# Performance work log

Hardware: AMD Instinct MI355X
Metric: run time of the kernel (lower is better)

The kernel has to match this reference:

```python
import jax, jax.numpy as jnp
import numpy as np

K = 5
PAD = 2  # same-size output: pad = dilation*(k-1)/2


def _patches(x, k, pad):
    # x: [B, C, H, W] -> [B, C, k, k, H', W'] (matches torch F.unfold + view layout)
    B, C, H, W = x.shape
    p = jax.lax.conv_general_dilated_patches(
        x, (k, k), (1, 1), [(pad, pad), (pad, pad)])
    return p.reshape(B, C, k, k, p.shape[-2], p.shape[-1])


def setup_inputs() -> dict:
    key = jax.random.key(0)
    k1, k2, k3, k4 = jax.random.split(key, 4)
    B, Cin, Cout, Cg, H, W = 4, 32, 32, 8, 128, 128
    x = jax.random.normal(k1, (B, Cin, H, W), jnp.float32)
    guide = jax.random.normal(k2, (B, Cg, H, W), jnp.float32)
    weight = jax.random.normal(k3, (Cout, Cin, K, K), jnp.float32) * 0.05
    bias = jax.random.normal(k4, (Cout,), jnp.float32) * 0.05
    return {"x": x, "guide": guide, "weight": weight, "bias": bias}


def reference(x, guide, weight, bias):
    k = weight.shape[-1]
    # --- packernel2d (gaussian, smooth_kernel_type='none', channel_wise=False) ---
    gp = _patches(guide, k, PAD)                      # [B, Cg, k, k, H, W]
    center = gp[:, :, k // 2, k // 2][:, :, None, None]  # self-tap feature
    d = gp - center
    kernel = jnp.exp(-0.5 * jnp.sum(d * d, axis=1, keepdims=True))  # [B,1,k,k,H,W]
    # --- pacconv2d native path ---
    cols = _patches(x, k, PAD)                        # [B, Cin, k, k, H, W]
    out = jnp.einsum('bjklmn,ojkl->bomn', cols * kernel, weight)
    return out + bias[None, :, None, None]
```

## Files before the change

kernel.cpp:

```cpp
#include <hip/hip_runtime.h>

#define Bn   4
#define CIN  32
#define COUT 32
#define CG   8
#define Hh   128
#define Ww   128
#define KK   5
#define HW   (Hh * Ww)

#define TW   64
#define TH   4
#define PRW  68
#define PRH  8
#define NSLOT (PRW * PRH)

#define PADW 132

typedef _Float16 h8  __attribute__((ext_vector_type(8)));
typedef _Float16 h2  __attribute__((ext_vector_type(2)));
typedef float    f4  __attribute__((ext_vector_type(4)));

#define XOFF  0
#define XJG   8704
#define WOFF  34816
#define KOFF  60416
#define SMEMB 73216

#define XT_OFF 0
#define WT_OFF 4460544
#define GT_OFF 4511744
#define WS_NEED 5560320

#define GLDS(gp, lp) __builtin_amdgcn_global_load_lds( \
    (const __attribute__((address_space(1))) void*)(gp), \
    (__attribute__((address_space(3))) void*)(lp), 16, 0, 0)

__global__ __launch_bounds__(512) void prep(
    const float* __restrict__ x, const float* __restrict__ guide,
    const float* __restrict__ w,
    _Float16* __restrict__ xt, _Float16* __restrict__ wt, _Float16* __restrict__ gt)
{
    const int bid = blockIdx.x;
    const int tid = threadIdx.x;

    if (bid < 512) {
        const int b = bid >> 7, m = bid & 127;
        const int n = tid & 127, jh = tid >> 7;
        const float* xp = x + ((size_t)(b * CIN + jh * 8)) * HW + m * Ww + n;
        h8 v;
#pragma unroll
        for (int e = 0; e < 8; ++e) v[e] = (_Float16)xp[(size_t)e * HW];
        ((h8*)xt)[(((size_t)b * PADW + m + 2) * PADW + n + 2) * 4 + jh] = v;
    } else if (bid < 562) {
        const int idx = (bid - 512) * 512 + tid;
        const int ht = idx >> 9;
        const int half = ht / 25, t = ht - half * 25;
        const int rem = idx & 511;
        const int jg = rem >> 7, o = (rem >> 3) & 15, e = rem & 7;
        wt[idx] = (_Float16)w[(size_t)(half * 16 + o) * (CIN * KK * KK) + (jg * 8 + e) * (KK * KK) + t];
    } else if (bid < 690) {
        const int gr = (bid - 562) * 4 + (tid >> 7);
        const int b = gr >> 7, m = gr & 127;
        const int n = tid & 127;
        const float* gp = guide + ((size_t)b * CG) * HW + m * Ww + n;
        h8 v;
#pragma unroll
        for (int e = 0; e < 8; ++e) v[e] = (_Float16)gp[(size_t)e * HW];
        ((h8*)gt)[(size_t)b * HW + m * Ww + n] = v;
    } else {
        const int idx = (bid - 690) * 512 + tid;
        if (idx < 4160) {
            const int b = idx / 1040, r = idx - b * 1040;
            int mp, np;
            if (r < 528) {
                const int mr = r / 132;
                mp = (mr < 2) ? mr : mr + 128;
                np = r - mr * 132;
            } else {
                const int r2 = r - 528;
                mp = 2 + (r2 >> 2);
                const int q = r2 & 3;
                np = (q < 2) ? q : q + 128;
            }
            h8 z = {};
            h8* dst = (h8*)xt + (((size_t)b * PADW + mp) * PADW + np) * 4;
            dst[0] = z; dst[1] = z; dst[2] = z; dst[3] = z;
        }
    }
}

__global__ __launch_bounds__(512, 2) void pac_mfma10(
    const _Float16* __restrict__ xt, const _Float16* __restrict__ wt,
    const _Float16* __restrict__ gt, const float* __restrict__ bias,
    float* __restrict__ out)
{
    __shared__ __align__(16) unsigned char smem[SMEMB];

    const int tid = threadIdx.x;
    const int bx  = blockIdx.x;
    const int bz  = blockIdx.y;
    const int tm = (bx >> 1) * TH;
    const int tn = (bx & 1) * TW;

    const int lane = tid & 63;
    const int l15 = lane & 15, kg = lane >> 4;
    const int wv = tid >> 6;

    for (int c = wv; c < 34; c += 8) {
        const int i = c * 64 + lane;
        const int jg = i / NSLOT;
        const int slot = i - jg * NSLOT;
        const int r = slot / PRW, cc = slot - r * PRW;
        const _Float16* g = xt +
            ((((size_t)bz * PADW + tm + r) * PADW + tn + cc) * 4 + jg) * 8;
        GLDS(g, smem + XOFF + c * 1024);
    }

    for (int c = wv; c < 25; c += 8) {
        const _Float16* g = wt + (c * 64 + lane) * 8;
        GLDS(g, smem + WOFF + c * 1024);
    }

    const h8* wh1 = (const h8*)wt + 1600;
    h8 B1r[25];
#pragma unroll
    for (int t = 0; t < 25; ++t)
        B1r[t] = wh1[t * 64 + kg * 16 + l15];

    {
        const int px = tid & 255, th = tid >> 8;
        const int pr = px >> 6, pc = px & 63;
        const int pg = px >> 5, ps = (px >> 4) & 1, pi = px & 15;
        const int m = tm + pr, n = tn + pc;
        const h8* gtb = (const h8*)gt + (size_t)bz * HW;
        const h8 c8 = gtb[m * Ww + n];
        float cg[8];
#pragma unroll
        for (int i = 0; i < 8; ++i) cg[i] = (float)c8[i];
        int t = 0;
#pragma unroll
        for (int k = 0; k < KK; ++k) {
#pragma unroll
            for (int l = 0; l < KK; ++l) {
                if ((t < 13) == (th == 0)) {
                    const int gm = m + k - 2, gn = n + l - 2;
                    h8 gv = {};
                    if ((unsigned)gm < (unsigned)Hh && (unsigned)gn < (unsigned)Ww)
                        gv = gtb[gm * Ww + gn];
                    float ss = 0.f;
#pragma unroll
                    for (int i = 0; i < 8; ++i) {
                        const float d = (float)gv[i] - cg[i];
                        ss = fmaf(d, d, ss);
                    }
                    *(_Float16*)(smem + KOFF + t * 512 + ((pg * 16 + pi) * 2 + ps) * 2) =
                        (_Float16)__expf(-0.5f * ss);
                }
                ++t;
            }
        }
    }

    __syncthreads();

    const int st0 = wv * 32, st1 = st0 + 16;
    const int r0 = wv >> 1;
    const int c00 = (wv & 1) * 32;

    f4 acc00 = {0.f,0.f,0.f,0.f}, acc01 = {0.f,0.f,0.f,0.f};
    f4 acc10 = {0.f,0.f,0.f,0.f}, acc11 = {0.f,0.f,0.f,0.f};
    const unsigned char* xg = smem + XOFF + kg * XJG;
    const int kbase = KOFF + (wv * 16 + l15) * 4;

    int t = 0;
#pragma unroll
    for (int k = 0; k < KK; ++k) {
#pragma unroll
        for (int l = 0; l < KK; ++l) {
            const int abase = ((r0 + k) * PRW + c00 + l + l15) * 16;
            h8 A0 = *(const h8*)(xg + abase);
            h8 A1 = *(const h8*)(xg + abase + 256);
            h8 B0 = *(const h8*)(smem + WOFF + t * 1024 + kg * 256 + l15 * 16);
            h2 kk = *(const h2*)(smem + kbase + t * 512);

            h8 A0s = A0 * kk[0];
            h8 A1s = A1 * kk[1];

            acc00 = __builtin_amdgcn_mfma_f32_16x16x32_f16(A0s, B0,     acc00, 0, 0, 0);
            acc01 = __builtin_amdgcn_mfma_f32_16x16x32_f16(A0s, B1r[t], acc01, 0, 0, 0);
            acc10 = __builtin_amdgcn_mfma_f32_16x16x32_f16(A1s, B0,     acc10, 0, 0, 0);
            acc11 = __builtin_amdgcn_mfma_f32_16x16x32_f16(A1s, B1r[t], acc11, 0, 0, 0);
            ++t;
        }
    }

    const float bv0 = bias[l15], bv1 = bias[16 + l15];
#pragma unroll
    for (int i = 0; i < 4; ++i) {
        acc00[i] += bv0; acc10[i] += bv0;
        acc01[i] += bv1; acc11[i] += bv1;
    }

    __syncthreads();
    float* outst = (float*)smem;
    *(f4*)(outst + l15 * 260 + st0 + kg * 4) = acc00;
    *(f4*)(outst + l15 * 260 + st1 + kg * 4) = acc10;
    *(f4*)(outst + (16 + l15) * 260 + st0 + kg * 4) = acc01;
    *(f4*)(outst + (16 + l15) * 260 + st1 + kg * 4) = acc11;
    __syncthreads();

    const int o = tid >> 4;
    const int i = tid & 15;
    float* op = out + ((size_t)(bz * COUT + o)) * HW;
#pragma unroll
    for (int c = 0; c < 4; ++c) {
        f4 v = *(const f4*)(outst + o * 260 + c * 64 + i * 4);
        *(f4*)(op + (size_t)(tm + c) * Ww + tn + i * 4) = v;
    }
}

typedef _Float16 h4v __attribute__((ext_vector_type(4)));
__global__ __launch_bounds__(512, 4) void pac_mfma2(
    const float* __restrict__ x, const float* __restrict__ guide,
    const float* __restrict__ weight, const float* __restrict__ bias,
    float* __restrict__ out)
{
    __shared__ __align__(16) unsigned char smem[SMEMB];
    const int tid  = threadIdx.x;
    const int bx   = blockIdx.x;
    const int half = blockIdx.y;
    const int bz   = blockIdx.z;
    const int tm = (bx >> 1) * TH;
    const int tn = (bx & 1) * TW;

    const float* xb = x + (size_t)bz * CIN * HW;
#pragma unroll
    for (int it = 0; it < 34; ++it) {
        const int idx  = it * 512 + tid;
        const int j    = idx / NSLOT;
        const int slot = idx - j * NSLOT;
        const int r    = slot / PRW;
        const int c    = slot - r * PRW;
        const int gm = tm + r - 2, gn = tn + c - 2;
        float v = 0.f;
        if ((unsigned)gm < (unsigned)Hh && (unsigned)gn < (unsigned)Ww)
            v = xb[(size_t)j * HW + gm * Ww + gn];
        *(_Float16*)(smem + XOFF + (j >> 3) * XJG + slot * 16 + (j & 7) * 2) = (_Float16)v;
    }
#pragma unroll
    for (int it = 0; it < 25; ++it) {
        const int idx = it * 512 + tid;
        const int o = idx & 15;
        const int j = (idx >> 4) & 31;
        const int t = idx >> 9;
        const float v = weight[(size_t)(half * 16 + o) * (CIN * KK * KK) + j * (KK * KK) + t];
        *(_Float16*)(smem + WOFF + t * 1024 + (j >> 3) * 256 + o * 16 + (j & 7) * 2) = (_Float16)v;
    }
    {
        const int px = tid & 255, th = tid >> 8;
        const int pr = px >> 6, pc = px & 63;
        const int m = tm + pr, n = tn + pc;
        const float* gb = guide + ((size_t)bz * CG) * HW + m * Ww + n;
        float center[CG];
#pragma unroll
        for (int c = 0; c < CG; ++c) center[c] = gb[c * HW];
        int t = 0;
#pragma unroll
        for (int k = 0; k < KK; ++k) {
            const int dm = k - 2;
            const bool rowok = ((unsigned)(m + dm) < (unsigned)Hh);
#pragma unroll
            for (int l = 0; l < KK; ++l) {
                if ((t < 13) == (th == 0)) {
                    const int dn = l - 2;
                    const bool ok = rowok && ((unsigned)(n + dn) < (unsigned)Ww);
                    float ss = 0.f;
#pragma unroll
                    for (int c = 0; c < CG; ++c) {
                        float gv = ok ? gb[c * HW + dm * Ww + dn] : 0.f;
                        float d = gv - center[c];
                        ss = fmaf(d, d, ss);
                    }
                    *(_Float16*)(smem + KOFF + t * 512 + px * 2) = (_Float16)__expf(-0.5f * ss);
                }
                ++t;
            }
        }
    }
    __syncthreads();
    const int lane = tid & 63;
    const int l15 = lane & 15, kg = lane >> 4;
    const int wv = tid >> 6;
    const int st0 = wv * 32, st1 = st0 + 16;
    const int r0 = wv >> 1;
    const int c00 = (wv & 1) * 32;
    f4 acc0 = {0.f, 0.f, 0.f, 0.f}, acc1 = {0.f, 0.f, 0.f, 0.f};
    const unsigned char* xg = smem + XOFF + kg * XJG;
    const float bv = bias[half * 16 + l15];
    int t = 0;
#pragma unroll
    for (int k = 0; k < KK; ++k) {
#pragma unroll
        for (int l = 0; l < KK; ++l) {
            const int abase = ((r0 + k) * PRW + c00 + l + l15) * 16;
            h8 A0 = *(const h8*)(xg + abase);
            h8 A1 = *(const h8*)(xg + abase + 256);
            h8 Bv = *(const h8*)(smem + WOFF + t * 1024 + kg * 256 + l15 * 16);
            f4 p0 = __builtin_amdgcn_mfma_f32_16x16x32_f16(A0, Bv, (f4){0.f,0.f,0.f,0.f}, 0, 0, 0);
            f4 p1 = __builtin_amdgcn_mfma_f32_16x16x32_f16(A1, Bv, (f4){0.f,0.f,0.f,0.f}, 0, 0, 0);
            h4v k0 = *(const h4v*)(smem + KOFF + t * 512 + (st0 + kg * 4) * 2);
            h4v k1 = *(const h4v*)(smem + KOFF + t * 512 + (st1 + kg * 4) * 2);
#pragma unroll
            for (int i = 0; i < 4; ++i) {
                acc0[i] = fmaf((float)k0[i], p0[i], acc0[i]);
                acc1[i] = fmaf((float)k1[i], p1[i], acc1[i]);
            }
            ++t;
        }
    }
#pragma unroll
    for (int i = 0; i < 4; ++i) { acc0[i] += bv; acc1[i] += bv; }
    __syncthreads();
    float* outst = (float*)smem;
    *(f4*)(outst + l15 * 260 + st0 + kg * 4) = acc0;
    *(f4*)(outst + l15 * 260 + st1 + kg * 4) = acc1;
    __syncthreads();
    const int o = tid >> 5;
    const int p = (tid & 31) * 8;
    f4 v0 = *(const f4*)(outst + o * 260 + p);
    f4 v1 = *(const f4*)(outst + o * 260 + p + 4);
    const int mr = p >> 6, nc = p & 63;
    float* op = out + ((size_t)(bz * COUT + half * 16 + o)) * HW + (size_t)(tm + mr) * Ww + tn + nc;
    *(f4*)op = v0;
    *(f4*)(op + 4) = v1;
}

extern "C" void kernel_launch(void* const* d_in, const int* in_sizes, int n_in,
                              void* d_out, int out_size, void* d_ws, size_t ws_size,
                              hipStream_t stream) {
    const float* x      = (const float*)d_in[0];
    const float* guide  = (const float*)d_in[1];
    const float* weight = (const float*)d_in[2];
    const float* bias   = (const float*)d_in[3];
    float* out = (float*)d_out;

    if (ws_size >= (size_t)WS_NEED) {
        _Float16* xt = (_Float16*)((char*)d_ws + XT_OFF);
        _Float16* wt = (_Float16*)((char*)d_ws + WT_OFF);
        _Float16* gt = (_Float16*)((char*)d_ws + GT_OFF);
        prep<<<dim3(699), 512, 0, stream>>>(x, guide, weight, xt, wt, gt);
        pac_mfma10<<<dim3(64, Bn), 512, 0, stream>>>(xt, wt, gt, bias, out);
    } else {
        pac_mfma2<<<dim3(64, 2, Bn), 512, 0, stream>>>(x, guide, weight, bias, out);
    }
}
```

Before: 23.57 us.

## Double block to 1024 threads with one 16-pixel tile per wave

The main fused kernel now runs 16 waves per block instead of 8. Each wave computes one 16-pixel by 32-output tile (two MFMAs per tap) instead of a 32-pixel tile with four MFMAs. Both weight halves are now staged in LDS rather than the second half being held in 25 registers per lane, and the gaussian kernel computation is split across four thread groups. The aim is to cut register pressure and raise the number of waves available to hide latency. The cost is larger LDS use per block (about 99KB), which may limit residency to one block per CU, and weight reads now come from LDS instead of registers.

```diff
diff --git a/kernel.cpp b/kernel.cpp
--- a/kernel.cpp
+++ b/kernel.cpp
@@ -18,14 +18,13 @@
 #define PADW 132
 
 typedef _Float16 h8  __attribute__((ext_vector_type(8)));
-typedef _Float16 h2  __attribute__((ext_vector_type(2)));
 typedef float    f4  __attribute__((ext_vector_type(4)));
 
 #define XOFF  0
 #define XJG   8704
 #define WOFF  34816
-#define KOFF  60416
-#define SMEMB 73216
+#define KOFF  86016
+#define SMEMB 98816
 
 #define XT_OFF 0
 #define WT_OFF 4460544
@@ -90,7 +89,7 @@
     }
 }
 
-__global__ __launch_bounds__(512, 2) void pac_mfma10(
+__global__ __launch_bounds__(1024, 4) void pac_mfma11(
     const _Float16* __restrict__ xt, const _Float16* __restrict__ wt,
     const _Float16* __restrict__ gt, const float* __restrict__ bias,
     float* __restrict__ out)
@@ -107,7 +106,7 @@
     const int l15 = lane & 15, kg = lane >> 4;
     const int wv = tid >> 6;
 
-    for (int c = wv; c < 34; c += 8) {
+    for (int c = wv; c < 34; c += 16) {
         const int i = c * 64 + lane;
         const int jg = i / NSLOT;
         const int slot = i - jg * NSLOT;
@@ -117,21 +116,15 @@
         GLDS(g, smem + XOFF + c * 1024);
     }
 
-    for (int c = wv; c < 25; c += 8) {
+    for (int c = wv; c < 50; c += 16) {
         const _Float16* g = wt + (c * 64 + lane) * 8;
         GLDS(g, smem + WOFF + c * 1024);
     }
 
-    const h8* wh1 = (const h8*)wt + 1600;
-    h8 B1r[25];
-#pragma unroll
-    for (int t = 0; t < 25; ++t)
-        B1r[t] = wh1[t * 64 + kg * 16 + l15];
-
     {
         const int px = tid & 255, th = tid >> 8;
+        const int lo = (th * 25) >> 2, hi = ((th + 1) * 25) >> 2;
         const int pr = px >> 6, pc = px & 63;
-        const int pg = px >> 5, ps = (px >> 4) & 1, pi = px & 15;
         const int m = tm + pr, n = tn + pc;
         const h8* gtb = (const h8*)gt + (size_t)bz * HW;
         const h8 c8 = gtb[m * Ww + n];
@@ -143,7 +136,7 @@
         for (int k = 0; k < KK; ++k) {
 #pragma unroll
             for (int l = 0; l < KK; ++l) {
-                if ((t < 13) == (th == 0)) {
+                if (t >= lo && t < hi) {
                     const int gm = m + k - 2, gn = n + l - 2;
                     h8 gv = {};
                     if ((unsigned)gm < (unsigned)Hh && (unsigned)gn < (unsigned)Ww)
@@ -154,7 +147,7 @@
                         const float d = (float)gv[i] - cg[i];
                         ss = fmaf(d, d, ss);
                     }
-                    *(_Float16*)(smem + KOFF + t * 512 + ((pg * 16 + pi) * 2 + ps) * 2) =
+                    *(_Float16*)(smem + KOFF + t * 512 + px * 2) =
                         (_Float16)__expf(-0.5f * ss);
                 }
                 ++t;
@@ -164,69 +157,62 @@
 
     __syncthreads();
 
-    const int st0 = wv * 32, st1 = st0 + 16;
-    const int r0 = wv >> 1;
-    const int c00 = (wv & 1) * 32;
-
-    f4 acc00 = {0.f,0.f,0.f,0.f}, acc01 = {0.f,0.f,0.f,0.f};
-    f4 acc10 = {0.f,0.f,0.f,0.f}, acc11 = {0.f,0.f,0.f,0.f};
+    const int st0 = wv * 16;
+    const int r0 = wv >> 2;
+    const int c0 = (wv & 3) * 16;
+
+    f4 acc0 = {0.f,0.f,0.f,0.f}, acc1 = {0.f,0.f,0.f,0.f};
     const unsigned char* xg = smem + XOFF + kg * XJG;
-    const int kbase = KOFF + (wv * 16 + l15) * 4;
 
     int t = 0;
 #pragma unroll
     for (int k = 0; k < KK; ++k) {
 #pragma unroll
         for (int l = 0; l < KK; ++l) {
-            const int abase = ((r0 + k) * PRW + c00 + l + l15) * 16;
+            const int abase = ((r0 + k) * PRW + c0 + l + l15) * 16;
             h8 A0 = *(const h8*)(xg + abase);
-            h8 A1 = *(const h8*)(xg + abase + 256);
             h8 B0 = *(const h8*)(smem + WOFF + t * 1024 + kg * 256 + l15 * 16);
-            h2 kk = *(const h2*)(smem + kbase + t * 512);
-
-            h8 A0s = A0 * kk[0];
-            h8 A1s = A1 * kk[1];
-
-            acc00 = __builtin_amdgcn_mfma_f32_16x16x32_f16(A0s, B0,     acc00, 0, 0, 0);
-            acc01 = __builtin_amdgcn_mfma_f32_16x16x32_f16(A0s, B1r[t], acc01, 0, 0, 0);
-            acc10 = __builtin_amdgcn_mfma_f32_16x16x32_f16(A1s, B0,     acc10, 0, 0, 0);
-            acc11 = __builtin_amdgcn_mfma_f32_16x16x32_f16(A1s, B1r[t], acc11, 0, 0, 0);
+            h8 B1 = *(const h8*)(smem + WOFF + 25600 + t * 1024 + kg * 256 + l15 * 16);
+            const _Float16 kk = *(const _Float16*)(smem + KOFF + t * 512 + (st0 + l15) * 2);
+
+            h8 A0s = A0 * kk;
+
+            acc0 = __builtin_amdgcn_mfma_f32_16x16x32_f16(A0s, B0, acc0, 0, 0, 0);
+            acc1 = __builtin_amdgcn_mfma_f32_16x16x32_f16(A0s, B1, acc1, 0, 0, 0);
             ++t;
         }
     }
 
     const float bv0 = bias[l15], bv1 = bias[16 + l15];
 #pragma unroll
-    for (int i = 0; i < 4; ++i) {
-        acc00[i] += bv0; acc10[i] += bv0;
-        acc01[i] += bv1; acc11[i] += bv1;
-    }
+    for (int i = 0; i < 4; ++i) { acc0[i] += bv0; acc1[i] += bv1; }
 
     __syncthreads();
     float* outst = (float*)smem;
-    *(f4*)(outst + l15 * 260 + st0 + kg * 4) = acc00;
-    *(f4*)(outst + l15 * 260 + st1 + kg * 4) = acc10;
-    *(f4*)(outst + (16 + l15) * 260 + st0 + kg * 4) = acc01;
-    *(f4*)(outst + (16 + l15) * 260 + st1 + kg * 4) = acc11;
-    __syncthreads();
-
-    const int o = tid >> 4;
-    const int i = tid & 15;
-    float* op = out + ((size_t)(bz * COUT + o)) * HW;
-#pragma unroll
-    for (int c = 0; c < 4; ++c) {
-        f4 v = *(const f4*)(outst + o * 260 + c * 64 + i * 4);
-        *(f4*)(op + (size_t)(tm + c) * Ww + tn + i * 4) = v;
-    }
+    *(f4*)(outst + l15 * 260 + st0 + kg * 4) = acc0;
+    *(f4*)(outst + (16 + l15) * 260 + st0 + kg * 4) = acc1;
+    __syncthreads();
+
+    const int o = tid >> 5;
+    const int p = (tid & 31) * 8;
+    const int row = p >> 6, col = p & 63;
+    float* op = out + ((size_t)(bz * COUT + o)) * HW + (size_t)(tm + row) * Ww + tn + col;
+    const float* src = outst + o * 260 + p;
+    *(f4*)op = *(const f4*)src;
+    *(f4*)(op + 4) = *(const f4*)(src + 4);
 }
 
 typedef _Float16 h4v __attribute__((ext_vector_type(4)));
+#define FXOFF  0
+#define FXJG   8704
+#define FWOFF  34816
+#define FKOFF  60416
 __global__ __launch_bounds__(512, 4) void pac_mfma2(
     const float* __restrict__ x, const float* __restrict__ guide,
     const float* __restrict__ weight, const float* __restrict__ bias,
     float* __restrict__ out)
 {
-    __shared__ __align__(16) unsigned char smem[SMEMB];
+    __shared__ __align__(16) unsigned char smem[73216];
     const int tid  = threadIdx.x;
     const int bx   = blockIdx.x;
     const int half = blockIdx.y;
@@ -246,7 +232,7 @@
         float v = 0.f;
         if ((unsigned)gm < (unsigned)Hh && (unsigned)gn < (unsigned)Ww)
             v = xb[(size_t)j * HW + gm * Ww + gn];
-        *(_Float16*)(smem + XOFF + (j >> 3) * XJG + slot * 16 + (j & 7) * 2) = (_Float16)v;
+        *(_Float16*)(smem + FXOFF + (j >> 3) * FXJG + slot * 16 + (j & 7) * 2) = (_Float16)v;
     }
 #pragma unroll
     for (int it = 0; it < 25; ++it) {
@@ -255,7 +241,7 @@
         const int j = (idx >> 4) & 31;
         const int t = idx >> 9;
         const float v = weight[(size_t)(half * 16 + o) * (CIN * KK * KK) + j * (KK * KK) + t];
-        *(_Float16*)(smem + WOFF + t * 1024 + (j >> 3) * 256 + o * 16 + (j & 7) * 2) = (_Float16)v;
+        *(_Float16*)(smem + FWOFF + t * 1024 + (j >> 3) * 256 + o * 16 + (j & 7) * 2) = (_Float16)v;
     }
     {
         const int px = tid & 255, th = tid >> 8;
@@ -282,7 +268,7 @@
                         float d = gv - center[c];
                         ss = fmaf(d, d, ss);
                     }
-                    *(_Float16*)(smem + KOFF + t * 512 + px * 2) = (_Float16)__expf(-0.5f * ss);
+                    *(_Float16*)(smem + FKOFF + t * 512 + px * 2) = (_Float16)__expf(-0.5f * ss);
                 }
                 ++t;
             }
@@ -296,7 +282,7 @@
     const int r0 = wv >> 1;
     const int c00 = (wv & 1) * 32;
     f4 acc0 = {0.f, 0.f, 0.f, 0.f}, acc1 = {0.f, 0.f, 0.f, 0.f};
-    const unsigned char* xg = smem + XOFF + kg * XJG;
+    const unsigned char* xg = smem + FXOFF + kg * FXJG;
     const float bv = bias[half * 16 + l15];
     int t = 0;
 #pragma unroll
@@ -306,11 +292,11 @@
             const int abase = ((r0 + k) * PRW + c00 + l + l15) * 16;
             h8 A0 = *(const h8*)(xg + abase);
             h8 A1 = *(const h8*)(xg + abase + 256);
-            h8 Bv = *(const h8*)(smem + WOFF + t * 1024 + kg * 256 + l15 * 16);
+            h8 Bv = *(const h8*)(smem + FWOFF + t * 1024 + kg * 256 + l15 * 16);
             f4 p0 = __builtin_amdgcn_mfma_f32_16x16x32_f16(A0, Bv, (f4){0.f,0.f,0.f,0.f}, 0, 0, 0);
             f4 p1 = __builtin_amdgcn_mfma_f32_16x16x32_f16(A1, Bv, (f4){0.f,0.f,0.f,0.f}, 0, 0, 0);
-            h4v k0 = *(const h4v*)(smem + KOFF + t * 512 + (st0 + kg * 4) * 2);
-            h4v k1 = *(const h4v*)(smem + KOFF + t * 512 + (st1 + kg * 4) * 2);
+            h4v k0 = *(const h4v*)(smem + FKOFF + t * 512 + (st0 + kg * 4) * 2);
+            h4v k1 = *(const h4v*)(smem + FKOFF + t * 512 + (st1 + kg * 4) * 2);
 #pragma unroll
             for (int i = 0; i < 4; ++i) {
                 acc0[i] = fmaf((float)k0[i], p0[i], acc0[i]);
@@ -350,7 +336,7 @@
         _Float16* wt = (_Float16*)((char*)d_ws + WT_OFF);
         _Float16* gt = (_Float16*)((char*)d_ws + GT_OFF);
         prep<<<dim3(699), 512, 0, stream>>>(x, guide, weight, xt, wt, gt);
-        pac_mfma10<<<dim3(64, Bn), 512, 0, stream>>>(xt, wt, gt, bias, out);
+        pac_mfma11<<<dim3(64, Bn), 1024, 0, stream>>>(xt, wt, gt, bias, out);
     } else {
         pac_mfma2<<<dim3(64, 2, Bn), 512, 0, stream>>>(x, guide, weight, bias, out);
     }
```

Measured after the change: 23.42 us. About the same (-0.6%).
